# Optimization experiments

Measured on AMD Instinct MI355X. Metric: run time of the kernel, lower is better.

## Reference

```python
import jax, jax.numpy as jnp
import numpy as np

B, T, D, H = 8, 2048, 1024, 1024

def setup_inputs() -> dict:
    key = jax.random.key(0)
    k1, k2, k3, k4 = jax.random.split(key, 4)
    scale = 1.0 / np.sqrt(D)
    return {
        "x": jax.random.normal(k1, (B, T, D), dtype=jnp.float32),
        "Wq": jax.random.normal(k2, (D, H), dtype=jnp.float32) * scale,
        "Wk": jax.random.normal(k3, (D, H), dtype=jnp.float32) * scale,
        "Wv": jax.random.normal(k4, (D, H), dtype=jnp.float32) * scale,
    }

def reference(x, Wq, Wk, Wv):
    # Single-head causal self-attention (dropout in eval mode = identity)
    q = jnp.einsum('btd,dh->bth', x, Wq)
    k = jnp.einsum('btd,dh->bth', x, Wk)
    v = jnp.einsum('btd,dh->bth', x, Wv)
    inv_sqrt_h = 1.0 / jnp.sqrt(jnp.asarray(q.shape[-1], q.dtype))
    scores = jnp.einsum('bqh,bkh->bqk', q, k) * inv_sqrt_h  # [B, T, T]
    Tq = scores.shape[-1]
    causal = jnp.tril(jnp.ones((Tq, Tq), dtype=bool))
    scores = jnp.where(causal, scores, jnp.asarray(-jnp.inf, scores.dtype))
    weights = jax.nn.softmax(scores, axis=-1)
    return jnp.einsum('bqk,bkh->bqh', weights, v)
```

## Files before the change

kernel.cpp:

```cpp
#include <hip/hip_runtime.h>

#define Bn 8
#define Tn 2048
#define Dn 1024
#define Hn 1024
#define Mn (Bn * Tn)

typedef __attribute__((ext_vector_type(8))) short bf16x8;
typedef __attribute__((ext_vector_type(4))) short short4v;
typedef __attribute__((ext_vector_type(16))) float f32x16;
typedef __attribute__((ext_vector_type(4))) float f32x4;

__device__ __forceinline__ unsigned short f2bf(float f) {
  union { float f; unsigned int u; } v; v.f = f;
  unsigned int u = v.u;
  u += 0x7FFFu + ((u >> 16) & 1u);
  return (unsigned short)(u >> 16);
}
__device__ __forceinline__ float bf2f(unsigned short h) {
  union { unsigned int u; float f; } v; v.u = ((unsigned int)h) << 16;
  return v.f;
}

__device__ __forceinline__ void gload_lds16(const unsigned short* g, unsigned short* l) {
  __builtin_amdgcn_global_load_lds((const __attribute__((address_space(1))) void*)g,
                                   (__attribute__((address_space(3))) void*)l, 16, 0, 0);
}


__device__ __forceinline__ void stage128x32s(const unsigned short* gbase, size_t row_stride,
                                             unsigned short* lds, int wave, int lane) {
#pragma unroll
  for (int c = 0; c < 2; ++c) {
    int rl = c * 16 + (lane >> 2);
    int pos = (lane & 3) ^ (rl & 3) ^ ((rl >> 2) & 3);
    const unsigned short* g = gbase + (size_t)(wave * 32 + rl) * row_stride + pos * 8;
    gload_lds16(g, lds + (wave * 32 + c * 16) * 32);
  }
}
__device__ __forceinline__ void stage128x64s(const unsigned short* gbase, size_t row_stride,
                                             unsigned short* lds0, unsigned short* lds1,
                                             int wave, int lane) {
  stage128x32s(gbase, row_stride, lds0, wave, lane);
  stage128x32s(gbase + 32, row_stride, lds1, wave, lane);
}

__device__ __forceinline__ void stage256x32s(const unsigned short* gbase, size_t row_stride,
                                             unsigned short* lds, int wave, int lane) {
#pragma unroll
  for (int c = 0; c < 2; ++c) {
    int rl = c * 16 + (lane >> 2);
    int pos = (lane & 3) ^ (rl & 3) ^ ((rl >> 2) & 3);
    const unsigned short* g = gbase + (size_t)(wave * 32 + rl) * row_stride + pos * 8;
    gload_lds16(g, lds + (wave * 32 + c * 16) * 32);
  }
}

__device__ __forceinline__ void mma_bk32(const unsigned short* lA, const unsigned short* lB,
                                         int wr, int wc, int l32, int half,
                                         f32x16 acc[2][2]) {
#pragma unroll
  for (int kk = 0; kk < 2; ++kk) {
    const int pos = (kk * 2 + half) ^ (l32 & 3) ^ ((l32 >> 2) & 3);
    bf16x8 af[2], bfr[2];
#pragma unroll
    for (int m = 0; m < 2; ++m)
      af[m] = *(const bf16x8*)&lA[(wr + m * 32 + l32) * 32 + pos * 8];
#pragma unroll
    for (int n = 0; n < 2; ++n)
      bfr[n] = *(const bf16x8*)&lB[(wc + n * 32 + l32) * 32 + pos * 8];
#pragma unroll
    for (int m = 0; m < 2; ++m)
#pragma unroll
      for (int n = 0; n < 2; ++n)
        acc[m][n] = __builtin_amdgcn_mfma_f32_32x32x16_bf16(af[m], bfr[n], acc[m][n], 0, 0, 0);
  }
}

__device__ __forceinline__ void rd4(const unsigned short* p, int rbase, int rl15, int csw,
                                    bf16x8 fr[4]) {
#pragma unroll
  for (int m = 0; m < 4; ++m)
    fr[m] = *(const bf16x8*)&p[(rbase + m * 16 + rl15) * 32 + csw * 8];
}

__device__ __forceinline__ void mm16(const bf16x8 af[4], const bf16x8 bf[4], f32x4 ap[][4]) {
  __builtin_amdgcn_s_setprio(1);
#pragma unroll
  for (int m = 0; m < 4; ++m)
#pragma unroll
    for (int n = 0; n < 4; ++n)
      ap[m][n] = __builtin_amdgcn_mfma_f32_16x16x32_bf16(af[m], bf[n], ap[m][n], 0, 0, 0);
  __builtin_amdgcn_s_setprio(0);
}

#define QKV_BAR  __builtin_amdgcn_s_barrier()
#define QKV_LGKM asm volatile("s_waitcnt lgkmcnt(0)" ::: "memory")
#define QKV_VM6  asm volatile("s_waitcnt vmcnt(6)" ::: "memory")
#define QKV_VM0  asm volatile("s_waitcnt vmcnt(0)" ::: "memory")

__global__ __launch_bounds__(256) void k_convert(const float* __restrict__ in,
                                                 unsigned short* __restrict__ out, int n4) {
  int idx = blockIdx.x * 256 + threadIdx.x;
  if (idx >= n4) return;
  float4 v = ((const float4*)in)[idx];
  short4v o;
  o.x = (short)f2bf(v.x); o.y = (short)f2bf(v.y);
  o.z = (short)f2bf(v.z); o.w = (short)f2bf(v.w);
  *(short4v*)(out + (size_t)idx * 4) = o;
}

__global__ __launch_bounds__(256) void k_cvt_w_t(const float* __restrict__ W0,
                                                 const float* __restrict__ W1,
                                                 const float* __restrict__ W2,
                                                 unsigned short* __restrict__ Wt3) {
  const int n0 = blockIdx.x * 64, k0 = blockIdx.y * 64, w = blockIdx.z;
  const float* W = (w == 0) ? W0 : (w == 1) ? W1 : W2;
  unsigned short* Wt = Wt3 + (size_t)w * Hn * Dn;
  __shared__ unsigned short lT[64 * 65];
  const int tid = threadIdx.x;
#pragma unroll
  for (int p = 0; p < 2; ++p) {
    int o = tid + p * 256;
    int r = o >> 3, c = (o & 7) * 8;
    const float* src = W + (size_t)(k0 + r) * Hn + n0 + c;
    float4 v0 = *(const float4*)src;
    float4 v1 = *(const float4*)(src + 4);
    unsigned short* d = &lT[r * 65 + c];
    d[0] = f2bf(v0.x); d[1] = f2bf(v0.y); d[2] = f2bf(v0.z); d[3] = f2bf(v0.w);
    d[4] = f2bf(v1.x); d[5] = f2bf(v1.y); d[6] = f2bf(v1.z); d[7] = f2bf(v1.w);
  }
  __syncthreads();
#pragma unroll
  for (int p = 0; p < 2; ++p) {
    int o = tid + p * 256;
    int r2 = o >> 3, c2 = (o & 7) * 8;
    bf16x8 v;
#pragma unroll
    for (int s = 0; s < 8; ++s) v[s] = (short)lT[(c2 + s) * 65 + r2];
    *(bf16x8*)(Wt + (size_t)(n0 + r2) * Dn + k0 + c2) = v;
  }
}

__global__ __launch_bounds__(512, 2) void gemm_qkv(const unsigned short* __restrict__ A,
                                                   const unsigned short* __restrict__ Wt3,
                                                   unsigned short* __restrict__ Q,
                                                   unsigned short* __restrict__ Kb,
                                                   unsigned short* __restrict__ Vt) {
  const int f = blockIdx.x;
  const int c = f & 7;
  const int q = f >> 3;
  const int nn = q % 12;
  const int w = nn >> 2;
  const int n0 = (nn & 3) * 256;
  const int m0 = ((q / 12) * 8 + c) * 256;
  const unsigned short* Bw = Wt3 + (size_t)w * Hn * Dn;
  __shared__ unsigned short lds[2][4][256 * 32];
  const int tid = threadIdx.x;
  const int lane = tid & 63, wave = tid >> 6;
  const int wr = (wave >> 2) * 128;
  const int wc = (wave & 3) * 64;
  const int rl15 = lane & 15, l4 = lane >> 4;
  const int csw = (l4 ^ (lane & 3) ^ ((lane >> 2) & 3)) & 3;

  f32x4 acc[8][4];
#pragma unroll
  for (int m = 0; m < 8; ++m)
#pragma unroll
    for (int n = 0; n < 4; ++n) acc[m][n] = (f32x4)(0.f);

  const unsigned short* Ab = A + (size_t)m0 * Dn;
  const unsigned short* Bb = Bw + (size_t)n0 * Dn;

  unsigned short* L0AL = &lds[0][0][0];
  unsigned short* L0AH = &lds[0][1][0];
  unsigned short* L0BL = &lds[0][2][0];
  unsigned short* L0BH = &lds[0][3][0];
  unsigned short* L1AL = &lds[1][0][0];
  unsigned short* L1AH = &lds[1][1][0];
  unsigned short* L1BL = &lds[1][2][0];
  unsigned short* L1BH = &lds[1][3][0];

  stage256x32s(Ab +  0, Dn, L0AL, wave, lane);
  stage256x32s(Bb +  0, Dn, L0BL, wave, lane);
  stage256x32s(Ab + 32, Dn, L0AH, wave, lane);
  stage256x32s(Bb + 32, Dn, L0BH, wave, lane);
  stage256x32s(Bb + 64, Dn, L1BL, wave, lane);
  stage256x32s(Ab + 64, Dn, L1AL, wave, lane);
  stage256x32s(Bb + 96, Dn, L1BH, wave, lane);
  QKV_VM6;
  QKV_BAR;

  bf16x8 af[4], bf[4];
#pragma unroll 1
  for (int i = 0; i < 7; ++i) {
    const int t1 = 2 * i + 1, t2 = 2 * i + 2, t3 = 2 * i + 3;
    rd4(L0AL, wr, rl15, csw, af);
    rd4(L0BL, wc, rl15, csw, bf);
    stage256x32s(Ab + t1 * 64 + 32, Dn, L1AH, wave, lane);
    QKV_BAR; QKV_LGKM; mm16(af, bf, &acc[0]); QKV_BAR;
    rd4(L0AL, wr + 64, rl15, csw, af);
    stage256x32s(Bb + t2 * 64, Dn, L0BL, wave, lane);
    QKV_BAR; QKV_LGKM; mm16(af, bf, &acc[4]); QKV_BAR;
    rd4(L0AH, wr, rl15, csw, af);
    rd4(L0BH, wc, rl15, csw, bf);
    stage256x32s(Ab + t2 * 64, Dn, L0AL, wave, lane);
    QKV_BAR; QKV_LGKM; mm16(af, bf, &acc[0]); QKV_BAR;
    rd4(L0AH, wr + 64, rl15, csw, af);
    stage256x32s(Bb + t2 * 64 + 32, Dn, L0BH, wave, lane);
    QKV_VM6;
    QKV_BAR; QKV_LGKM; mm16(af, bf, &acc[4]); QKV_BAR;
    rd4(L1AL, wr, rl15, csw, af);
    rd4(L1BL, wc, rl15, csw, bf);
    stage256x32s(Ab + t2 * 64 + 32, Dn, L0AH, wave, lane);
    QKV_BAR; QKV_LGKM; mm16(af, bf, &acc[0]); QKV_BAR;
    rd4(L1AL, wr + 64, rl15, csw, af);
    stage256x32s(Bb + t3 * 64, Dn, L1BL, wave, lane);
    QKV_BAR; QKV_LGKM; mm16(af, bf, &acc[4]); QKV_BAR;
    rd4(L1AH, wr, rl15, csw, af);
    rd4(L1BH, wc, rl15, csw, bf);
    stage256x32s(Ab + t3 * 64, Dn, L1AL, wave, lane);
    QKV_BAR; QKV_LGKM; mm16(af, bf, &acc[0]); QKV_BAR;
    rd4(L1AH, wr + 64, rl15, csw, af);
    stage256x32s(Bb + t3 * 64 + 32, Dn, L1BH, wave, lane);
    QKV_VM6;
    QKV_BAR; QKV_LGKM; mm16(af, bf, &acc[4]); QKV_BAR;
  }
  rd4(L0AL, wr, rl15, csw, af);
  rd4(L0BL, wc, rl15, csw, bf);
  stage256x32s(Ab + 15 * 64 + 32, Dn, L1AH, wave, lane);
  QKV_BAR; QKV_LGKM; mm16(af, bf, &acc[0]); QKV_BAR;
  rd4(L0AL, wr + 64, rl15, csw, af);
  QKV_BAR; QKV_LGKM; mm16(af, bf, &acc[4]); QKV_BAR;
  rd4(L0AH, wr, rl15, csw, af);
  rd4(L0BH, wc, rl15, csw, bf);
  QKV_BAR; QKV_LGKM; mm16(af, bf, &acc[0]); QKV_BAR;
  rd4(L0AH, wr + 64, rl15, csw, af);
  QKV_VM0;
  QKV_BAR; QKV_LGKM; mm16(af, bf, &acc[4]); QKV_BAR;
  rd4(L1AL, wr, rl15, csw, af);
  rd4(L1BL, wc, rl15, csw, bf);
  QKV_BAR; QKV_LGKM; mm16(af, bf, &acc[0]); QKV_BAR;
  rd4(L1AL, wr + 64, rl15, csw, af);
  QKV_BAR; QKV_LGKM; mm16(af, bf, &acc[4]); QKV_BAR;
  rd4(L1AH, wr, rl15, csw, af);
  rd4(L1BH, wc, rl15, csw, bf);
  QKV_BAR; QKV_LGKM; mm16(af, bf, &acc[0]); QKV_BAR;
  rd4(L1AH, wr + 64, rl15, csw, af);
  QKV_LGKM; mm16(af, bf, &acc[4]);

  if (w != 2) {
    unsigned short* Cp = (w == 0) ? Q : Kb;
#pragma unroll
    for (int m = 0; m < 8; ++m) {
      const int row = m0 + wr + m * 16 + l4 * 4;
#pragma unroll
      for (int n = 0; n < 4; ++n) {
        const int col = n0 + wc + n * 16 + rl15;
#pragma unroll
        for (int r = 0; r < 4; ++r)
          Cp[(size_t)(row + r) * Hn + col] = f2bf(acc[m][n][r]);
      }
    }
  } else {
    const int bb = m0 >> 11;
    const int tb = m0 & 2047;
#pragma unroll
    for (int m = 0; m < 8; ++m) {
      const int t0 = tb + wr + m * 16 + l4 * 4;
#pragma unroll
      for (int n = 0; n < 4; ++n) {
        const int h = n0 + wc + n * 16 + rl15;
        short4v o;
        o.x = (short)f2bf(acc[m][n][0]);
        o.y = (short)f2bf(acc[m][n][1]);
        o.z = (short)f2bf(acc[m][n][2]);
        o.w = (short)f2bf(acc[m][n][3]);
        *(short4v*)(Vt + ((size_t)bb * Hn + h) * Tn + t0) = o;
      }
    }
  }
}

__global__ __launch_bounds__(256) void gemm_scores(const unsigned short* __restrict__ Q,
                                                   const unsigned short* __restrict__ K,
                                                   unsigned short* __restrict__ S) {
  const int f = blockIdx.x;
  const int b = f & 7;
  const int q = f >> 3;
  const int rt = 15 - (q & 15);
  const int ct = q >> 4;
  if (ct > rt) return;
  const int j0 = ct * 128, i0 = rt * 128;
  const unsigned short* Qb = Q + (size_t)b * Tn * Hn;
  const unsigned short* Kp = K + (size_t)b * Tn * Hn;
  unsigned short* Sb = S + (size_t)b * Tn * Tn;
  __shared__ unsigned short lA[2][128 * 32];
  __shared__ unsigned short lB[2][128 * 32];
  const int tid = threadIdx.x;
  const int lane = tid & 63, wave = tid >> 6;
  const int wr = (wave >> 1) * 64, wc = (wave & 1) * 64;
  const int l32 = lane & 31, half = lane >> 5;

  f32x16 acc[2][2];
#pragma unroll
  for (int m = 0; m < 2; ++m)
#pragma unroll
    for (int n = 0; n < 2; ++n) acc[m][n] = (f32x16)(0.f);

  for (int kt = 0; kt < Hn / 64; ++kt) {
    stage128x64s(Qb + (size_t)i0 * Hn + kt * 64, Hn, lA[0], lA[1], wave, lane);
    stage128x64s(Kp + (size_t)j0 * Hn + kt * 64, Hn, lB[0], lB[1], wave, lane);
    __syncthreads();
    mma_bk32(lA[0], lB[0], wr, wc, l32, half, acc);
    mma_bk32(lA[1], lB[1], wr, wc, l32, half, acc);
    __syncthreads();
  }
#pragma unroll
  for (int m = 0; m < 2; ++m)
#pragma unroll
    for (int n = 0; n < 2; ++n) {
      int col = j0 + wc + n * 32 + l32;
#pragma unroll
      for (int qd = 0; qd < 4; ++qd) {
        int rb = i0 + wr + m * 32 + 8 * qd + 4 * half;
#pragma unroll
        for (int rr = 0; rr < 4; ++rr) {
          int row = rb + rr;
          float e = (col <= row) ? __expf(acc[m][n][qd * 4 + rr] * 0.03125f) : 0.f;
          Sb[(size_t)row * Tn + col] = f2bf(e);
        }
      }
    }
}

__global__ __launch_bounds__(256) void k_rowsum(const unsigned short* __restrict__ S,
                                                float* __restrict__ l) {
  const int b = blockIdx.y;
  const int i = blockIdx.x * 4 + (threadIdx.x >> 6);
  const int lane = threadIdx.x & 63;
  const unsigned short* row = S + ((size_t)b * Tn + i) * (size_t)Tn;
  const int npad = ((i >> 7) + 1) << 7;
  float s = 0.f;
  for (int j0 = 0; j0 < npad; j0 += 512) {
    int j = j0 + lane * 8;
    if (j < npad) {
      bf16x8 v = *(const bf16x8*)(row + j);
#pragma unroll
      for (int t = 0; t < 8; ++t) s += bf2f((unsigned short)v[t]);
    }
  }
#pragma unroll
  for (int off = 32; off > 0; off >>= 1) s += __shfl_down(s, off);
  if (lane == 0) l[(size_t)b * Tn + i] = s;
}

__global__ __launch_bounds__(256) void gemm_out(const unsigned short* __restrict__ P,
                                                const unsigned short* __restrict__ Vt,
                                                const float* __restrict__ lbuf,
                                                float* __restrict__ O) {
  const int f = blockIdx.x;
  const int b = f & 7;
  const int q = f >> 3;
  const int n0 = (q & 7) * 128;
  const int rt = 15 - (q >> 3);
  const int i0 = rt * 128;
  const int nkt = (rt + 1) * 2;
  const unsigned short* Pb = P + (size_t)b * Tn * Tn;
  const unsigned short* Vb = Vt + (size_t)b * Tn * Hn;
  __shared__ unsigned short lA[2][128 * 32];
  __shared__ unsigned short lB[2][128 * 32];
  const int tid = threadIdx.x;
  const int lane = tid & 63, wave = tid >> 6;
  const int wr = (wave >> 1) * 64, wc = (wave & 1) * 64;
  const int l32 = lane & 31, half = lane >> 5;

  f32x16 acc[2][2];
#pragma unroll
  for (int m = 0; m < 2; ++m)
#pragma unroll
    for (int n = 0; n < 2; ++n) acc[m][n] = (f32x16)(0.f);

  for (int kt = 0; kt < nkt; ++kt) {
    stage128x64s(Pb + (size_t)i0 * Tn + kt * 64, Tn, lA[0], lA[1], wave, lane);
    stage128x64s(Vb + (size_t)n0 * Tn + kt * 64, Tn, lB[0], lB[1], wave, lane);
    __syncthreads();
    mma_bk32(lA[0], lB[0], wr, wc, l32, half, acc);
    mma_bk32(lA[1], lB[1], wr, wc, l32, half, acc);
    __syncthreads();
  }
#pragma unroll
  for (int m = 0; m < 2; ++m)
#pragma unroll
    for (int n = 0; n < 2; ++n) {
      int col = n0 + wc + n * 32 + l32;
#pragma unroll
      for (int qd = 0; qd < 4; ++qd) {
        int rb = i0 + wr + m * 32 + 8 * qd + 4 * half;
        float4 lv = *(const float4*)&lbuf[(size_t)b * Tn + rb];
#pragma unroll
        for (int rr = 0; rr < 4; ++rr) {
          float inv = 1.f / ((&lv.x)[rr]);
          O[((size_t)b * Tn + rb + rr) * Hn + col] = acc[m][n][qd * 4 + rr] * inv;
        }
      }
    }
}

extern "C" void kernel_launch(void* const* d_in, const int* in_sizes, int n_in,
                              void* d_out, int out_size, void* d_ws, size_t ws_size,
                              hipStream_t stream) {
  const float* x  = (const float*)d_in[0];
  const float* Wq = (const float*)d_in[1];
  const float* Wk = (const float*)d_in[2];
  const float* Wv = (const float*)d_in[3];
  float* out = (float*)d_out;

  char* ws = (char*)d_ws;
  const size_t MiB = 1024 * 1024;
  unsigned short* Wt3 = (unsigned short*)(ws + 0 * MiB);
  unsigned short* xb  = (unsigned short*)(ws + 6 * MiB);
  unsigned short* Qb  = (unsigned short*)(ws + 38 * MiB);
  unsigned short* Kb  = (unsigned short*)(ws + 70 * MiB);
  unsigned short* Vt  = (unsigned short*)(ws + 102 * MiB);
  unsigned short* S   = (unsigned short*)(ws + 134 * MiB);
  float*          lrow = (float*)(ws + 6 * MiB);

  {
    int n4 = (Mn * Dn) / 4;
    k_convert<<<dim3(n4 / 256), 256, 0, stream>>>(x, xb, n4);
  }
  {
    dim3 g(Hn / 64, Dn / 64, 3);
    k_cvt_w_t<<<g, 256, 0, stream>>>(Wq, Wk, Wv, Wt3);
  }
  {
    gemm_qkv<<<dim3(768), 512, 0, stream>>>(xb, Wt3, Qb, Kb, Vt);
  }
  {
    gemm_scores<<<dim3(2048), 256, 0, stream>>>(Qb, Kb, S);
  }
  {
    k_rowsum<<<dim3(Tn / 4, Bn), 256, 0, stream>>>(S, lrow);
  }
  {
    gemm_out<<<dim3(1024), 256, 0, stream>>>(S, Vt, lrow, out);
  }
}
```

Baseline: 334.2 us.

## Restructure QKV GEMM pipeline to 32-MFMA phases with paired A/B staging

After: 348.1 us. +4.2%, slower.

```diff
diff --git a/kernel.cpp b/kernel.cpp
--- a/kernel.cpp
+++ b/kernel.cpp
@@ -84,19 +84,10 @@
     fr[m] = *(const bf16x8*)&p[(rbase + m * 16 + rl15) * 32 + csw * 8];
 }
 
-__device__ __forceinline__ void mm16(const bf16x8 af[4], const bf16x8 bf[4], f32x4 ap[][4]) {
-  __builtin_amdgcn_s_setprio(1);
-#pragma unroll
-  for (int m = 0; m < 4; ++m)
-#pragma unroll
-    for (int n = 0; n < 4; ++n)
-      ap[m][n] = __builtin_amdgcn_mfma_f32_16x16x32_bf16(af[m], bf[n], ap[m][n], 0, 0, 0);
-  __builtin_amdgcn_s_setprio(0);
-}
-
 #define QKV_BAR  __builtin_amdgcn_s_barrier()
 #define QKV_LGKM asm volatile("s_waitcnt lgkmcnt(0)" ::: "memory")
-#define QKV_VM6  asm volatile("s_waitcnt vmcnt(6)" ::: "memory")
+#define QKV_VM8  asm volatile("s_waitcnt vmcnt(8)" ::: "memory")
+#define QKV_VM4  asm volatile("s_waitcnt vmcnt(4)" ::: "memory")
 #define QKV_VM0  asm volatile("s_waitcnt vmcnt(0)" ::: "memory")
 
 __global__ __launch_bounds__(256) void k_convert(const float* __restrict__ in,
@@ -181,73 +172,82 @@
   unsigned short* L1BL = &lds[1][2][0];
   unsigned short* L1BH = &lds[1][3][0];
 
+  bf16x8 a0[4], a1[4], b0[4];
+  auto RP = [&](const unsigned short* pa, const unsigned short* pb) {
+    rd4(pa, wr, rl15, csw, a0);
+    rd4(pa, wr + 64, rl15, csw, a1);
+    rd4(pb, wc, rl15, csw, b0);
+  };
+  auto M32 = [&]() {
+    __builtin_amdgcn_s_setprio(1);
+#pragma unroll
+    for (int m = 0; m < 4; ++m)
+#pragma unroll
+      for (int n = 0; n < 4; ++n)
+        acc[m][n] = __builtin_amdgcn_mfma_f32_16x16x32_bf16(a0[m], b0[n], acc[m][n], 0, 0, 0);
+#pragma unroll
+    for (int m = 0; m < 4; ++m)
+#pragma unroll
+      for (int n = 0; n < 4; ++n)
+        acc[m + 4][n] = __builtin_amdgcn_mfma_f32_16x16x32_bf16(a1[m], b0[n], acc[m + 4][n], 0, 0, 0);
+    __builtin_amdgcn_s_setprio(0);
+  };
+
   stage256x32s(Ab +  0, Dn, L0AL, wave, lane);
   stage256x32s(Bb +  0, Dn, L0BL, wave, lane);
   stage256x32s(Ab + 32, Dn, L0AH, wave, lane);
   stage256x32s(Bb + 32, Dn, L0BH, wave, lane);
+  stage256x32s(Ab + 64, Dn, L1AL, wave, lane);
   stage256x32s(Bb + 64, Dn, L1BL, wave, lane);
-  stage256x32s(Ab + 64, Dn, L1AL, wave, lane);
-  stage256x32s(Bb + 96, Dn, L1BH, wave, lane);
-  QKV_VM6;
+  QKV_VM8;
   QKV_BAR;
 
-  bf16x8 af[4], bf[4];
 #pragma unroll 1
-  for (int i = 0; i < 7; ++i) {
-    const int t1 = 2 * i + 1, t2 = 2 * i + 2, t3 = 2 * i + 3;
-    rd4(L0AL, wr, rl15, csw, af);
-    rd4(L0BL, wc, rl15, csw, bf);
-    stage256x32s(Ab + t1 * 64 + 32, Dn, L1AH, wave, lane);
-    QKV_BAR; QKV_LGKM; mm16(af, bf, &acc[0]); QKV_BAR;
-    rd4(L0AL, wr + 64, rl15, csw, af);
-    stage256x32s(Bb + t2 * 64, Dn, L0BL, wave, lane);
-    QKV_BAR; QKV_LGKM; mm16(af, bf, &acc[4]); QKV_BAR;
-    rd4(L0AH, wr, rl15, csw, af);
-    rd4(L0BH, wc, rl15, csw, bf);
-    stage256x32s(Ab + t2 * 64, Dn, L0AL, wave, lane);
-    QKV_BAR; QKV_LGKM; mm16(af, bf, &acc[0]); QKV_BAR;
-    rd4(L0AH, wr + 64, rl15, csw, af);
-    stage256x32s(Bb + t2 * 64 + 32, Dn, L0BH, wave, lane);
-    QKV_VM6;
-    QKV_BAR; QKV_LGKM; mm16(af, bf, &acc[4]); QKV_BAR;
-    rd4(L1AL, wr, rl15, csw, af);
-    rd4(L1BL, wc, rl15, csw, bf);
-    stage256x32s(Ab + t2 * 64 + 32, Dn, L0AH, wave, lane);
-    QKV_BAR; QKV_LGKM; mm16(af, bf, &acc[0]); QKV_BAR;
-    rd4(L1AL, wr + 64, rl15, csw, af);
-    stage256x32s(Bb + t3 * 64, Dn, L1BL, wave, lane);
-    QKV_BAR; QKV_LGKM; mm16(af, bf, &acc[4]); QKV_BAR;
-    rd4(L1AH, wr, rl15, csw, af);
-    rd4(L1BH, wc, rl15, csw, bf);
-    stage256x32s(Ab + t3 * 64, Dn, L1AL, wave, lane);
-    QKV_BAR; QKV_LGKM; mm16(af, bf, &acc[0]); QKV_BAR;
-    rd4(L1AH, wr + 64, rl15, csw, af);
-    stage256x32s(Bb + t3 * 64 + 32, Dn, L1BH, wave, lane);
-    QKV_VM6;
-    QKV_BAR; QKV_LGKM; mm16(af, bf, &acc[4]); QKV_BAR;
-  }
-  rd4(L0AL, wr, rl15, csw, af);
-  rd4(L0BL, wc, rl15, csw, bf);
+  for (int i = 0; i < 6; ++i) {
+    const int s1 = 2 * i + 1, s2 = 2 * i + 2, s3 = 2 * i + 3;
+    RP(L0AL, L0BL);
+    stage256x32s(Ab + s1 * 64 + 32, Dn, L1AH, wave, lane);
+    stage256x32s(Bb + s1 * 64 + 32, Dn, L1BH, wave, lane);
+    QKV_VM8; QKV_BAR; QKV_LGKM; M32(); QKV_BAR;
+    RP(L0AH, L0BH);
+    stage256x32s(Ab + s2 * 64, Dn, L0AL, wave, lane);
+    stage256x32s(Bb + s2 * 64, Dn, L0BL, wave, lane);
+    QKV_VM8; QKV_BAR; QKV_LGKM; M32(); QKV_BAR;
+    RP(L1AL, L1BL);
+    stage256x32s(Ab + s2 * 64 + 32, Dn, L0AH, wave, lane);
+    stage256x32s(Bb + s2 * 64 + 32, Dn, L0BH, wave, lane);
+    QKV_VM8; QKV_BAR; QKV_LGKM; M32(); QKV_BAR;
+    RP(L1AH, L1BH);
+    stage256x32s(Ab + s3 * 64, Dn, L1AL, wave, lane);
+    stage256x32s(Bb + s3 * 64, Dn, L1BL, wave, lane);
+    QKV_VM8; QKV_BAR; QKV_LGKM; M32(); QKV_BAR;
+  }
+  RP(L0AL, L0BL);
+  stage256x32s(Ab + 13 * 64 + 32, Dn, L1AH, wave, lane);
+  stage256x32s(Bb + 13 * 64 + 32, Dn, L1BH, wave, lane);
+  QKV_VM8; QKV_BAR; QKV_LGKM; M32(); QKV_BAR;
+  RP(L0AH, L0BH);
+  stage256x32s(Ab + 14 * 64, Dn, L0AL, wave, lane);
+  stage256x32s(Bb + 14 * 64, Dn, L0BL, wave, lane);
+  QKV_VM8; QKV_BAR; QKV_LGKM; M32(); QKV_BAR;
+  RP(L1AL, L1BL);
+  stage256x32s(Ab + 14 * 64 + 32, Dn, L0AH, wave, lane);
+  stage256x32s(Bb + 14 * 64 + 32, Dn, L0BH, wave, lane);
+  QKV_VM8; QKV_BAR; QKV_LGKM; M32(); QKV_BAR;
+  RP(L1AH, L1BH);
+  stage256x32s(Ab + 15 * 64, Dn, L1AL, wave, lane);
+  stage256x32s(Bb + 15 * 64, Dn, L1BL, wave, lane);
+  QKV_VM8; QKV_BAR; QKV_LGKM; M32(); QKV_BAR;
+  RP(L0AL, L0BL);
   stage256x32s(Ab + 15 * 64 + 32, Dn, L1AH, wave, lane);
-  QKV_BAR; QKV_LGKM; mm16(af, bf, &acc[0]); QKV_BAR;
-  rd4(L0AL, wr + 64, rl15, csw, af);
-  QKV_BAR; QKV_LGKM; mm16(af, bf, &acc[4]); QKV_BAR;
-  rd4(L0AH, wr, rl15, csw, af);
-  rd4(L0BH, wc, rl15, csw, bf);
-  QKV_BAR; QKV_LGKM; mm16(af, bf, &acc[0]); QKV_BAR;
-  rd4(L0AH, wr + 64, rl15, csw, af);
-  QKV_VM0;
-  QKV_BAR; QKV_LGKM; mm16(af, bf, &acc[4]); QKV_BAR;
-  rd4(L1AL, wr, rl15, csw, af);
-  rd4(L1BL, wc, rl15, csw, bf);
-  QKV_BAR; QKV_LGKM; mm16(af, bf, &acc[0]); QKV_BAR;
-  rd4(L1AL, wr + 64, rl15, csw, af);
-  QKV_BAR; QKV_LGKM; mm16(af, bf, &acc[4]); QKV_BAR;
-  rd4(L1AH, wr, rl15, csw, af);
-  rd4(L1BH, wc, rl15, csw, bf);
-  QKV_BAR; QKV_LGKM; mm16(af, bf, &acc[0]); QKV_BAR;
-  rd4(L1AH, wr + 64, rl15, csw, af);
-  QKV_LGKM; mm16(af, bf, &acc[4]);
+  stage256x32s(Bb + 15 * 64 + 32, Dn, L1BH, wave, lane);
+  QKV_VM8; QKV_BAR; QKV_LGKM; M32(); QKV_BAR;
+  RP(L0AH, L0BH);
+  QKV_VM4; QKV_BAR; QKV_LGKM; M32(); QKV_BAR;
+  RP(L1AL, L1BL);
+  QKV_VM0; QKV_BAR; QKV_LGKM; M32(); QKV_BAR;
+  RP(L1AH, L1BH);
+  QKV_LGKM; M32();
 
   if (w != 2) {
     unsigned short* Cp = (w == 0) ? Q : Kb;
```
